# Performance work log

Measured on AMD Instinct MI355X. Metric: run time of the kernel, lower is better.

Reference implementation:

```python
import jax, jax.numpy as jnp
import numpy as np

D_STATE = 16

def setup_inputs() -> dict:
    key = jax.random.key(0)
    ks = jax.random.split(key, 7)
    B, L, d_model = 2, 4096, 1024
    d_inner, d_conv, d_state = 2048, 4, D_STATE
    s = 0.02
    return {
        "x": jax.random.normal(ks[0], (B, L, d_model), jnp.float32),
        "W_in": jax.random.normal(ks[1], (2 * d_inner, d_model), jnp.float32) * s,
        "conv_w": jax.random.normal(ks[2], (d_inner, d_conv), jnp.float32) * 0.3,
        "conv_b": jax.random.normal(ks[3], (d_inner,), jnp.float32) * 0.1,
        "W_xproj": jax.random.normal(ks[4], (2 * d_state + d_inner, d_inner), jnp.float32) * s,
        "D": jnp.ones((d_inner,), jnp.float32),
        "W_out": jax.random.normal(ks[5], (d_model, d_inner), jnp.float32) * s,
    }

def _silu(v):
    return v * jax.nn.sigmoid(v)

def reference(x, W_in, conv_w, conv_b, W_xproj, D, W_out):
    Bsz, L, _ = x.shape
    d_inner, d_conv = conv_w.shape
    d_state = D_STATE
    # in_proj -> split into x branch and gate z
    xz = jnp.einsum('bld,ed->ble', x, W_in)           # [B,L,2*d_inner]
    xb, z = xz[..., :d_inner], xz[..., d_inner:]
    # causal depthwise conv1d (left pad d_conv-1, truncate to L)
    xpad = jnp.pad(xb, ((0, 0), (d_conv - 1, 0), (0, 0)))
    xc = conv_b
    for k in range(d_conv):  # tiny fixed kernel loop
        xc = xc + conv_w[:, k] * xpad[:, k:k + L, :]
    xc = _silu(xc)                                    # [B,L,d_inner]
    # x_proj -> B, C, delta
    proj = jnp.einsum('bld,ed->ble', xc, W_xproj)     # [B,L,2*d_state+d_inner]
    Bm = proj[..., :d_state]
    Cm = proj[..., d_state:2 * d_state]
    delta = jax.nn.softplus(proj[..., 2 * d_state:])  # [B,L,d_inner]
    # selective 'scan' as written collapses: y[b,l,d] = delta*x * sum_s B*C + D*x
    bc = jnp.einsum('bls,bls->bl', Bm, Cm)            # [B,L]
    y = delta * xc * bc[..., None] + D * xc
    y = y * _silu(z)
    return jnp.einsum('bld,ed->ble', y, W_out)        # [B,L,d_model]
```

## Files before the change

### kernel.cpp

```cpp
#include <hip/hip_runtime.h>
#include <hip/hip_bf16.h>
#include <cstdint>
#include <cmath>

typedef __bf16 bf16x8 __attribute__((ext_vector_type(8)));
typedef float  f32x4  __attribute__((ext_vector_type(4)));
typedef unsigned short u16x8 __attribute__((ext_vector_type(8)));

#define BT 128
#define BK 64

__device__ __forceinline__ float bf2f(unsigned short h) {
  union { unsigned int u; float f; } v; v.u = ((unsigned int)h) << 16;
  return v.f;
}
__device__ __forceinline__ unsigned short f2bf(float x) {
  union { float f; unsigned int u; } v; v.f = x;
  unsigned int r = v.u + 0x7fffu + ((v.u >> 16) & 1u);
  return (unsigned short)(r >> 16);
}

__device__ __forceinline__ void gld_lds16(const void* g, void* l) {
  __builtin_amdgcn_global_load_lds(
      (const __attribute__((address_space(1))) unsigned int*)g,
      (__attribute__((address_space(3))) unsigned int*)l,
      16, 0, 0);
}

__device__ __forceinline__ void cvt4(const float* __restrict__ in,
                                     unsigned short* __restrict__ out, int i) {
  float4 v = reinterpret_cast<const float4*>(in)[i];
  ushort4 o;
  o.x = f2bf(v.x); o.y = f2bf(v.y); o.z = f2bf(v.z); o.w = f2bf(v.w);
  reinterpret_cast<ushort4*>(out)[i] = o;
}

__global__ void cvt_head(const float* __restrict__ x, unsigned short* __restrict__ xb,
                         const float* __restrict__ W_in, unsigned short* __restrict__ wb) {
  int b = blockIdx.x;
  if (b < 8192) cvt4(x, xb, b * 256 + threadIdx.x);
  else          cvt4(W_in, wb, (b - 8192) * 256 + threadIdx.x);
}

__device__ void conv_strip(const unsigned short* __restrict__ xz,
                           const float* __restrict__ conv_w,
                           const float* __restrict__ conv_b,
                           unsigned short* __restrict__ xc,
                           int strip, int tid) {
  const int bl0  = strip * 32;
  const int seq0 = bl0 & ~4095;
  const int c0   = tid * 8;
  float w[4][8], bb[8];
#pragma unroll
  for (int j = 0; j < 8; ++j) {
    float4 wr = reinterpret_cast<const float4*>(conv_w)[c0 + j];
    w[0][j] = wr.x; w[1][j] = wr.y; w[2][j] = wr.z; w[3][j] = wr.w;
    bb[j] = conv_b[c0 + j];
  }
  float win[3][8];
#pragma unroll
  for (int i = 0; i < 3; ++i) {
    int r = bl0 - 3 + i;
    if (r >= seq0) {
      u16x8 v = *reinterpret_cast<const u16x8*>(xz + (size_t)r * 4096 + c0);
#pragma unroll
      for (int j = 0; j < 8; ++j) win[i][j] = bf2f(v[j]);
    } else {
#pragma unroll
      for (int j = 0; j < 8; ++j) win[i][j] = 0.f;
    }
  }
  for (int i = 0; i < 32; ++i) {
    const int bl = bl0 + i;
    u16x8 v = *reinterpret_cast<const u16x8*>(xz + (size_t)bl * 4096 + c0);
    u16x8 o;
#pragma unroll
    for (int j = 0; j < 8; ++j) {
      float cur = bf2f(v[j]);
      float a = bb[j] + w[0][j] * win[0][j] + w[1][j] * win[1][j]
                      + w[2][j] * win[2][j] + w[3][j] * cur;
      o[j] = f2bf(a / (1.f + expf(-a)));
      win[0][j] = win[1][j]; win[1][j] = win[2][j]; win[2][j] = cur;
    }
    *reinterpret_cast<u16x8*>(xc + (size_t)bl * 2048 + c0) = o;
  }
}

__global__ void mid_fused(const unsigned short* __restrict__ xz,
                          const float* __restrict__ conv_w,
                          const float* __restrict__ conv_b,
                          unsigned short* __restrict__ xc,
                          const float* __restrict__ W_xproj, unsigned short* __restrict__ wx_bf,
                          const float* __restrict__ W_out,   unsigned short* __restrict__ wo_bf) {
  int b = blockIdx.x;
  if (b < 256) { conv_strip(xz, conv_w, conv_b, xc, b, threadIdx.x); return; }
  b -= 256;
  if (b < 4160) { cvt4(W_xproj, wx_bf, b * 256 + threadIdx.x); return; }
  cvt4(W_out, wo_bf, (b - 4160) * 256 + threadIdx.x);
}

template <int GUARD_N, int OUT_F32>
__global__ __launch_bounds__(256, 2)
void gemm_bt(const unsigned short* __restrict__ A,
             const unsigned short* __restrict__ B,
             void* __restrict__ Cv,
             int N, int K, int ldA, int ldB, int ldC)
{
  __shared__ __align__(16) unsigned short sA[BT * BK];
  __shared__ __align__(16) unsigned short sB[BT * BK];

  const int tid  = threadIdx.x;
  const int lane = tid & 63;
  const int wave = tid >> 6;
  const int row0 = blockIdx.x * BT;
  const int col0 = blockIdx.y * BT;

  const int wrow = (wave & 1) * 64;
  const int wcol = (wave >> 1) * 64;
  const int l15  = lane & 15;
  const int q    = lane >> 4;

  f32x4 acc[4][4];
#pragma unroll
  for (int i = 0; i < 4; ++i)
#pragma unroll
    for (int j = 0; j < 4; ++j)
      acc[i][j] = (f32x4){0.f, 0.f, 0.f, 0.f};

  const int nk = K / BK;
  for (int kt = 0; kt < nk; ++kt) {
    const int k0 = kt * BK;
#pragma unroll
    for (int t = 0; t < 4; ++t) {
      int c  = t * 256 + tid;
      int r  = c >> 3;
      int g  = c & 7;
      int gs = (g ^ (r & 7)) * 8;
      gld_lds16(A + (size_t)(row0 + r) * ldA + k0 + gs, (void*)(sA + c * 8));
      int br = col0 + r;
      if (GUARD_N) br = (br < N) ? br : (N - 1);
      gld_lds16(B + (size_t)br * ldB + k0 + gs, (void*)(sB + c * 8));
    }
    __syncthreads();

#pragma unroll
    for (int kk = 0; kk < BK; kk += 32) {
      const int grb = kk >> 3;
      bf16x8 af[4], bfr[4];
#pragma unroll
      for (int i = 0; i < 4; ++i) {
        int ar = wrow + i * 16 + l15;
        af[i] = *reinterpret_cast<const bf16x8*>(
            sA + ar * BK + (((grb + q) ^ (ar & 7)) << 3));
        int br = wcol + i * 16 + l15;
        bfr[i] = *reinterpret_cast<const bf16x8*>(
            sB + br * BK + (((grb + q) ^ (br & 7)) << 3));
      }
#pragma unroll
      for (int i = 0; i < 4; ++i)
#pragma unroll
        for (int j = 0; j < 4; ++j)
          acc[i][j] = __builtin_amdgcn_mfma_f32_16x16x32_bf16(af[i], bfr[j], acc[i][j], 0, 0, 0);
    }
    __syncthreads();
  }

#pragma unroll
  for (int i = 0; i < 4; ++i) {
#pragma unroll
    for (int j = 0; j < 4; ++j) {
      int colw = col0 + wcol + j * 16 + l15;
      if (GUARD_N && colw >= N) continue;
#pragma unroll
      for (int r = 0; r < 4; ++r) {
        int roww = row0 + wrow + i * 16 + q * 4 + r;
        if (OUT_F32)
          ((float*)Cv)[(size_t)roww * ldC + colw] = acc[i][j][r];
        else
          ((unsigned short*)Cv)[(size_t)roww * ldC + colw] = f2bf(acc[i][j][r]);
      }
    }
  }
}

#define BARX() do { __builtin_amdgcn_sched_barrier(0); \
                    __builtin_amdgcn_s_barrier(); \
                    __builtin_amdgcn_sched_barrier(0); } while (0)
#define VMW(n) asm volatile("s_waitcnt vmcnt(" #n ")" ::: "memory")

#define STAGE_A(b, h, kt) do { \
  const unsigned short* _p = Ab + (size_t)((h) * 128) * ldA + (kt) * 64; \
  gld_lds16(_p,                     (void*)&sA[b][((h) * 128      + rr) * 64 + (g8 << 3)]); \
  gld_lds16(_p + (size_t)64 * ldA,  (void*)&sA[b][((h) * 128 + 64 + rr) * 64 + (g8 << 3)]); \
} while (0)

#define STAGE_B(b, h, kt) do { \
  const unsigned short* _p = Bb + (size_t)((h) * 128) * ldB + (kt) * 64; \
  gld_lds16(_p,                     (void*)&sB[b][((h) * 128      + rr) * 64 + (g8 << 3)]); \
  gld_lds16(_p + (size_t)64 * ldB,  (void*)&sB[b][((h) * 128 + 64 + rr) * 64 + (g8 << 3)]); \
} while (0)

#define RD_A_SET(dst, b, p) do { \
  dst[0][0] = *reinterpret_cast<const bf16x8*>(&sA[b][aOff + (2*(p)    ) * 1024 + kph0]); \
  dst[0][1] = *reinterpret_cast<const bf16x8*>(&sA[b][aOff + (2*(p)    ) * 1024 + kph1]); \
  dst[1][0] = *reinterpret_cast<const bf16x8*>(&sA[b][aOff + (2*(p) + 1) * 1024 + kph0]); \
  dst[1][1] = *reinterpret_cast<const bf16x8*>(&sA[b][aOff + (2*(p) + 1) * 1024 + kph1]); \
} while (0)

#define RD_B_SET(dst, b) do { \
  dst[0][0] = *reinterpret_cast<const bf16x8*>(&sB[b][bOff + 0 * 1024 + kph0]); \
  dst[0][1] = *reinterpret_cast<const bf16x8*>(&sB[b][bOff + 0 * 1024 + kph1]); \
  dst[1][0] = *reinterpret_cast<const bf16x8*>(&sB[b][bOff + 1 * 1024 + kph0]); \
  dst[1][1] = *reinterpret_cast<const bf16x8*>(&sB[b][bOff + 1 * 1024 + kph1]); \
  dst[2][0] = *reinterpret_cast<const bf16x8*>(&sB[b][bOff + 2 * 1024 + kph0]); \
  dst[2][1] = *reinterpret_cast<const bf16x8*>(&sB[b][bOff + 2 * 1024 + kph1]); \
  dst[3][0] = *reinterpret_cast<const bf16x8*>(&sB[b][bOff + 3 * 1024 + kph0]); \
  dst[3][1] = *reinterpret_cast<const bf16x8*>(&sB[b][bOff + 3 * 1024 + kph1]); \
} while (0)

#define MMA(i, j, k, Af, Bf) \
  acc[i][j] = __builtin_amdgcn_mfma_f32_16x16x32_bf16(Af[(i) & 1][k], Bf[j][k], acc[i][j], 0, 0, 0)

#define MFMA_PH(p, Af, Bf) do { \
  __builtin_amdgcn_s_setprio(1); \
  MMA(2*(p),   0, 0, Af, Bf); MMA(2*(p),   1, 0, Af, Bf); \
  MMA(2*(p),   2, 0, Af, Bf); MMA(2*(p),   3, 0, Af, Bf); \
  MMA(2*(p)+1, 0, 0, Af, Bf); MMA(2*(p)+1, 1, 0, Af, Bf); \
  MMA(2*(p)+1, 2, 0, Af, Bf); MMA(2*(p)+1, 3, 0, Af, Bf); \
  MMA(2*(p),   0, 1, Af, Bf); MMA(2*(p),   1, 1, Af, Bf); \
  MMA(2*(p),   2, 1, Af, Bf); MMA(2*(p),   3, 1, Af, Bf); \
  MMA(2*(p)+1, 0, 1, Af, Bf); MMA(2*(p)+1, 1, 1, Af, Bf); \
  MMA(2*(p)+1, 2, 1, Af, Bf); MMA(2*(p)+1, 3, 1, Af, Bf); \
  __builtin_amdgcn_s_setprio(0); \
} while (0)

__global__ __launch_bounds__(512, 2)
void gemm256(const unsigned short* __restrict__ A,
             const unsigned short* __restrict__ B,
             unsigned short* __restrict__ C,
             int K, int ldA, int ldB, int ldC, int nbn)
{
  __shared__ __align__(16) unsigned short sA[2][256 * 64];
  __shared__ __align__(16) unsigned short sB[2][256 * 64];

  const int tid  = threadIdx.x;
  const int lane = tid & 63;
  const int wave = tid >> 6;
  const int wm = wave >> 2;
  const int wn = wave & 3;
  const int l15 = lane & 15;
  const int q   = lane >> 4;

  const int nwg = gridDim.x;
  const int wg  = blockIdx.x;
  const int swz = (wg & 7) * (nwg >> 3) + (wg >> 3);
  const int row0 = (swz / nbn) * 256;
  const int col0 = (swz % nbn) * 256;

  const int rr  = tid >> 3;
  const int g8  = tid & 7;
  const int gsw = ((g8 ^ (rr & 7)) << 3);
  const unsigned short* Ab = A + (size_t)(row0 + rr) * ldA + gsw;
  const unsigned short* Bb = B + (size_t)(col0 + rr) * ldB + gsw;

  const int aOff = (wm * 128 + l15) * 64;
  const int bOff = (wn * 64  + l15) * 64;
  const int a7   = l15 & 7;
  const int kph0 = ((q       ^ a7) << 3);
  const int kph1 = (((4 + q) ^ a7) << 3);

  f32x4 acc[8][4];
#pragma unroll
  for (int i = 0; i < 8; ++i)
#pragma unroll
    for (int j = 0; j < 4; ++j)
      acc[i][j] = (f32x4){0.f, 0.f, 0.f, 0.f};

  bf16x8 afe[2][2], afo[2][2];
  bf16x8 bfe[4][2], bfo[4][2];

  const int nk = K >> 6;
  STAGE_A(0, 0, 0); STAGE_A(0, 1, 0);
  STAGE_B(0, 0, 0); STAGE_B(0, 1, 0);
  STAGE_B(1, 0, 1); STAGE_B(1, 1, 1);
  VMW(4);
  BARX();
  RD_B_SET(bfe, 0); RD_A_SET(afe, 0, 0);

  const int niter = K >> 7;
  for (int it = 0; it < niter; ++it) {
    const int kt1 = 2 * it + 1;
    int ktE = 2 * it + 2; if (ktE > nk - 1) ktE = nk - 1;
    int ktO = 2 * it + 3; if (ktO > nk - 1) ktO = nk - 1;

    STAGE_A(1, 0, kt1);
    BARX();
    MFMA_PH(0, afe, bfe); RD_A_SET(afo, 0, 1);
    BARX();
    STAGE_A(1, 1, kt1);
    BARX();
    MFMA_PH(1, afo, bfe); RD_A_SET(afe, 0, 2);
    BARX();
    STAGE_B(0, 0, ktE);
    BARX();
    MFMA_PH(2, afe, bfe); RD_A_SET(afo, 0, 3);
    BARX();
    STAGE_B(0, 1, ktE);
    VMW(4);
    BARX();
    MFMA_PH(3, afo, bfe); RD_B_SET(bfo, 1); RD_A_SET(afe, 1, 0);
    BARX();

    STAGE_A(0, 0, ktE);
    BARX();
    MFMA_PH(0, afe, bfo); RD_A_SET(afo, 1, 1);
    BARX();
    STAGE_A(0, 1, ktE);
    BARX();
    MFMA_PH(1, afo, bfo); RD_A_SET(afe, 1, 2);
    BARX();
    STAGE_B(1, 0, ktO);
    BARX();
    MFMA_PH(2, afe, bfo); RD_A_SET(afo, 1, 3);
    BARX();
    STAGE_B(1, 1, ktO);
    VMW(4);
    BARX();
    MFMA_PH(3, afo, bfo); RD_B_SET(bfe, 0); RD_A_SET(afe, 0, 0);
    BARX();
  }

#pragma unroll
  for (int i = 0; i < 8; ++i) {
    const int roww = row0 + wm * 128 + i * 16 + q * 4;
#pragma unroll
    for (int j = 0; j < 4; ++j) {
      const int colw = col0 + wn * 64 + j * 16 + l15;
      unsigned short* cp = C + (size_t)roww * ldC + colw;
#pragma unroll
      for (int r = 0; r < 4; ++r)
        cp[(size_t)r * ldC] = f2bf(acc[i][j][r]);
    }
  }
}

__global__ __launch_bounds__(256)
void proj_strip(const unsigned short* __restrict__ xc,
                const unsigned short* __restrict__ wx,
                unsigned short* __restrict__ proj)
{
  __shared__ float red[4][32 * 32];
  const int tid  = threadIdx.x;
  const int lane = tid & 63;
  const int wave = tid >> 6;
  const int l15  = lane & 15;
  const int q    = lane >> 4;
  const int row0 = blockIdx.x * 32;

  f32x4 acc[2][2];
#pragma unroll
  for (int i = 0; i < 2; ++i)
#pragma unroll
    for (int j = 0; j < 2; ++j) acc[i][j] = (f32x4){0.f, 0.f, 0.f, 0.f};

  const int kbase = wave * 512;
#pragma unroll 4
  for (int kk = 0; kk < 512; kk += 32) {
    const int k = kbase + kk + q * 8;
    bf16x8 a0 = *reinterpret_cast<const bf16x8*>(&xc[(size_t)(row0 + l15) * 2048 + k]);
    bf16x8 a1 = *reinterpret_cast<const bf16x8*>(&xc[(size_t)(row0 + 16 + l15) * 2048 + k]);
    bf16x8 b0 = *reinterpret_cast<const bf16x8*>(&wx[(size_t)(l15) * 2048 + k]);
    bf16x8 b1 = *reinterpret_cast<const bf16x8*>(&wx[(size_t)(16 + l15) * 2048 + k]);
    acc[0][0] = __builtin_amdgcn_mfma_f32_16x16x32_bf16(a0, b0, acc[0][0], 0, 0, 0);
    acc[0][1] = __builtin_amdgcn_mfma_f32_16x16x32_bf16(a0, b1, acc[0][1], 0, 0, 0);
    acc[1][0] = __builtin_amdgcn_mfma_f32_16x16x32_bf16(a1, b0, acc[1][0], 0, 0, 0);
    acc[1][1] = __builtin_amdgcn_mfma_f32_16x16x32_bf16(a1, b1, acc[1][1], 0, 0, 0);
  }

#pragma unroll
  for (int i = 0; i < 2; ++i)
#pragma unroll
    for (int j = 0; j < 2; ++j)
#pragma unroll
      for (int r = 0; r < 4; ++r)
        red[wave][(i * 16 + q * 4 + r) * 32 + j * 16 + l15] = acc[i][j][r];
  __syncthreads();

#pragma unroll
  for (int t = 0; t < 4; ++t) {
    int idx = tid + t * 256;
    float s = red[0][idx] + red[1][idx] + red[2][idx] + red[3][idx];
    proj[(size_t)(row0 + (idx >> 5)) * 2080 + (idx & 31)] = f2bf(s);
  }
}

__global__ void gate_kernel(const unsigned short* __restrict__ proj,
                            const unsigned short* __restrict__ xz,
                            const float* __restrict__ Dw,
                            unsigned short* __restrict__ xc_y)
{
  const int bl = blockIdx.x;
  const unsigned short* p = proj + (size_t)bl * 2080;
  u16x8 pb0 = *reinterpret_cast<const u16x8*>(p);
  u16x8 pb1 = *reinterpret_cast<const u16x8*>(p + 8);
  u16x8 pc0 = *reinterpret_cast<const u16x8*>(p + 16);
  u16x8 pc1 = *reinterpret_cast<const u16x8*>(p + 24);
  float bc = 0.f;
#pragma unroll
  for (int s = 0; s < 8; ++s)
    bc += bf2f(pb0[s]) * bf2f(pc0[s]) + bf2f(pb1[s]) * bf2f(pc1[s]);

  const int c0 = threadIdx.x * 8;
  u16x8 dv  = *reinterpret_cast<const u16x8*>(p + 32 + c0);
  u16x8 xcv = *reinterpret_cast<const u16x8*>(xc_y + (size_t)bl * 2048 + c0);
  u16x8 zv  = *reinterpret_cast<const u16x8*>(xz + (size_t)bl * 4096 + 2048 + c0);
  float4 d0 = reinterpret_cast<const float4*>(Dw)[c0 / 4];
  float4 d1 = reinterpret_cast<const float4*>(Dw)[c0 / 4 + 1];
  const float* dd0 = reinterpret_cast<const float*>(&d0);
  const float* dd1 = reinterpret_cast<const float*>(&d1);

  u16x8 o;
#pragma unroll
  for (int j = 0; j < 8; ++j) {
    float d = bf2f(dv[j]);
    float delta = (d > 15.f) ? d : log1pf(expf(d));
    float xv = bf2f(xcv[j]);
    float z  = bf2f(zv[j]);
    float Dj = (j < 4) ? dd0[j] : dd1[j - 4];
    float y = delta * xv * bc + Dj * xv;
    y *= z / (1.f + expf(-z));
    o[j] = f2bf(y);
  }
  *reinterpret_cast<u16x8*>(xc_y + (size_t)bl * 2048 + c0) = o;
}

extern "C" void kernel_launch(void* const* d_in, const int* in_sizes, int n_in,
                              void* d_out, int out_size, void* d_ws, size_t ws_size,
                              hipStream_t stream) {
  const float* x       = (const float*)d_in[0];
  const float* W_in    = (const float*)d_in[1];
  const float* conv_w  = (const float*)d_in[2];
  const float* conv_b  = (const float*)d_in[3];
  const float* W_xproj = (const float*)d_in[4];
  const float* Dw      = (const float*)d_in[5];
  const float* W_out   = (const float*)d_in[6];
  float* out = (float*)d_out;

  unsigned short* xz_bf   = (unsigned short*)d_ws;
  unsigned short* xc_bf   = xz_bf  + (size_t)8192 * 4096;
  unsigned short* proj_bf = xc_bf  + (size_t)8192 * 2048;
  unsigned short* xb_bf   = proj_bf + (size_t)8192 * 2080;
  unsigned short* w_bf    = xb_bf  + (size_t)8192 * 1024;

  cvt_head<<<8192 + 4096, 256, 0, stream>>>(x, xb_bf, W_in, w_bf);
  gemm256<<<512, 512, 0, stream>>>(xb_bf, w_bf, xz_bf, 1024, 1024, 1024, 4096, 16);
  mid_fused<<<256 + 4160 + 2048, 256, 0, stream>>>(xz_bf, conv_w, conv_b, xc_bf,
                                                   W_xproj, xb_bf, W_out, w_bf);
  proj_strip<<<256, 256, 0, stream>>>(xc_bf, xb_bf, proj_bf);
  gemm256<<<256, 512, 0, stream>>>(xc_bf, xb_bf + (size_t)32 * 2048, proj_bf + 32,
                                   2048, 2048, 2048, 2080, 8);
  gate_kernel<<<8192, 256, 0, stream>>>(proj_bf, xz_bf, Dw, xc_bf);
  gemm_bt<0, 1><<<dim3(64, 8), 256, 0, stream>>>(xc_bf, w_bf, out, 1024, 2048, 2048, 2048, 1024);
}
```

Baseline: 398.7 us.

## Stage GEMM epilogue through LDS, remap tiles per XCD, use fast exp intrinsics

The 256x256 GEMM epilogue now writes bf16 results into shared memory and then stores full rows with 16-byte vector writes, replacing scattered 2-byte stores. The workgroup-to-tile mapping is changed so each of the 8 XCD groups owns a compact block of rows and columns, which should improve L2 reuse of A and B. The SiLU and softplus code switches to __expf/__logf, which is cheaper but slightly less accurate. The epilogue adds extra barriers and LDS round trips, and softplus computed as log(1+exp) loses some precision for small values.

```diff
diff --git a/kernel.cpp b/kernel.cpp
--- a/kernel.cpp
+++ b/kernel.cpp
@@ -79,7 +79,7 @@
       float cur = bf2f(v[j]);
       float a = bb[j] + w[0][j] * win[0][j] + w[1][j] * win[1][j]
                       + w[2][j] * win[2][j] + w[3][j] * cur;
-      o[j] = f2bf(a / (1.f + expf(-a)));
+      o[j] = f2bf(a / (1.f + __expf(-a)));
       win[0][j] = win[1][j]; win[1][j] = win[2][j]; win[2][j] = cur;
     }
     *reinterpret_cast<u16x8*>(xc + (size_t)bl * 2048 + c0) = o;
@@ -187,6 +187,7 @@
                     __builtin_amdgcn_s_barrier(); \
                     __builtin_amdgcn_sched_barrier(0); } while (0)
 #define VMW(n) asm volatile("s_waitcnt vmcnt(" #n ")" ::: "memory")
+#define LGKM0() asm volatile("s_waitcnt lgkmcnt(0)" ::: "memory")
 
 #define STAGE_A(b, h, kt) do { \
   const unsigned short* _p = Ab + (size_t)((h) * 128) * ldA + (kt) * 64; \
@@ -238,10 +239,11 @@
 void gemm256(const unsigned short* __restrict__ A,
              const unsigned short* __restrict__ B,
              unsigned short* __restrict__ C,
-             int K, int ldA, int ldB, int ldC, int nbn)
+             int K, int ldA, int ldB, int ldC, int ccsh)
 {
-  __shared__ __align__(16) unsigned short sA[2][256 * 64];
-  __shared__ __align__(16) unsigned short sB[2][256 * 64];
+  __shared__ __align__(16) unsigned short smem[4 * 256 * 64];
+  unsigned short (*sA)[256 * 64] = (unsigned short (*)[256 * 64])smem;
+  unsigned short (*sB)[256 * 64] = (unsigned short (*)[256 * 64])(smem + 2 * 256 * 64);
 
   const int tid  = threadIdx.x;
   const int lane = tid & 63;
@@ -253,9 +255,12 @@
 
   const int nwg = gridDim.x;
   const int wg  = blockIdx.x;
-  const int swz = (wg & 7) * (nwg >> 3) + (wg >> 3);
-  const int row0 = (swz / nbn) * 256;
-  const int col0 = (swz % nbn) * 256;
+  const int x   = wg & 7;
+  const int c   = wg >> 3;
+  const int CC  = 1 << ccsh;
+  const int R   = (nwg >> 3) >> ccsh;
+  const int row0 = ((x >> 1) * R + (c >> ccsh)) * 256;
+  const int col0 = ((x & 1) * CC + (c & (CC - 1))) * 256;
 
   const int rr  = tid >> 3;
   const int g8  = tid & 7;
@@ -330,16 +335,31 @@
     BARX();
   }
 
-#pragma unroll
-  for (int i = 0; i < 8; ++i) {
-    const int roww = row0 + wm * 128 + i * 16 + q * 4;
-#pragma unroll
-    for (int j = 0; j < 4; ++j) {
-      const int colw = col0 + wn * 64 + j * 16 + l15;
-      unsigned short* cp = C + (size_t)roww * ldC + colw;
-#pragma unroll
-      for (int r = 0; r < 4; ++r)
-        cp[(size_t)r * ldC] = f2bf(acc[i][j][r]);
+  VMW(0);
+  LGKM0();
+  BARX();
+  {
+    unsigned short* cs = smem;
+#pragma unroll
+    for (int i = 0; i < 8; ++i) {
+      const int row = wm * 128 + i * 16 + q * 4;
+#pragma unroll
+      for (int j = 0; j < 4; ++j) {
+        const int col = wn * 64 + j * 16 + l15;
+#pragma unroll
+        for (int r = 0; r < 4; ++r)
+          cs[(row + r) * 256 + col] = f2bf(acc[i][j][r]);
+      }
+    }
+    LGKM0();
+    BARX();
+#pragma unroll
+    for (int s = 0; s < 16; ++s) {
+      const int u   = s * 4096 + tid * 8;
+      const int row = u >> 8;
+      const int col = u & 255;
+      u16x8 v = *reinterpret_cast<const u16x8*>(&cs[u]);
+      *reinterpret_cast<u16x8*>(C + (size_t)(row0 + row) * ldC + col0 + col) = v;
     }
   }
 }
@@ -423,12 +443,12 @@
 #pragma unroll
   for (int j = 0; j < 8; ++j) {
     float d = bf2f(dv[j]);
-    float delta = (d > 15.f) ? d : log1pf(expf(d));
+    float delta = (d > 15.f) ? d : __logf(1.f + __expf(d));
     float xv = bf2f(xcv[j]);
     float z  = bf2f(zv[j]);
     float Dj = (j < 4) ? dd0[j] : dd1[j - 4];
     float y = delta * xv * bc + Dj * xv;
-    y *= z / (1.f + expf(-z));
+    y *= z / (1.f + __expf(-z));
     o[j] = f2bf(y);
   }
   *reinterpret_cast<u16x8*>(xc_y + (size_t)bl * 2048 + c0) = o;
@@ -453,12 +473,12 @@
   unsigned short* w_bf    = xb_bf  + (size_t)8192 * 1024;
 
   cvt_head<<<8192 + 4096, 256, 0, stream>>>(x, xb_bf, W_in, w_bf);
-  gemm256<<<512, 512, 0, stream>>>(xb_bf, w_bf, xz_bf, 1024, 1024, 1024, 4096, 16);
+  gemm256<<<512, 512, 0, stream>>>(xb_bf, w_bf, xz_bf, 1024, 1024, 1024, 4096, 3);
   mid_fused<<<256 + 4160 + 2048, 256, 0, stream>>>(xz_bf, conv_w, conv_b, xc_bf,
                                                    W_xproj, xb_bf, W_out, w_bf);
   proj_strip<<<256, 256, 0, stream>>>(xc_bf, xb_bf, proj_bf);
   gemm256<<<256, 512, 0, stream>>>(xc_bf, xb_bf + (size_t)32 * 2048, proj_bf + 32,
-                                   2048, 2048, 2048, 2080, 8);
+                                   2048, 2048, 2048, 2080, 2);
   gate_kernel<<<8192, 256, 0, stream>>>(proj_bf, xz_bf, Dw, xc_bf);
   gemm_bt<0, 1><<<dim3(64, 8), 256, 0, stream>>>(xc_bf, w_bf, out, 1024, 2048, 2048, 2048, 1024);
 }
```

After: 343.9 us. 1.16x faster.
